# Kernel tuning notes

Hardware: AMD Instinct MI355X
Metric: run time of the kernel (lower is better)

The kernel has to match this reference:

```python
import jax, jax.numpy as jnp
import numpy as np

MAX_REL = 64  # max_relative_position (init kwarg)


def setup_inputs() -> dict:
    B, S, D, K = 8, 2048, 256, MAX_REL
    key = jax.random.key(0)
    ks = jax.random.split(key, 12)
    scale = 0.02
    return {
        "repre": jax.random.normal(ks[0], (B, S, D), jnp.float32),
        "mask": jnp.ones((B, S), jnp.int32),
        "wq1": jax.random.normal(ks[1], (D, D), jnp.float32) * scale,
        "bq1": jnp.zeros((D,), jnp.float32),
        "wk1": jax.random.normal(ks[2], (D, D), jnp.float32) * scale,
        "bk1": jnp.zeros((D,), jnp.float32),
        "rel1": jax.random.normal(ks[3], (2 * K + 1, D), jnp.float32) * scale,
        "wq2": jax.random.normal(ks[4], (D, D), jnp.float32) * scale,
        "bq2": jnp.zeros((D,), jnp.float32),
        "wk2": jax.random.normal(ks[5], (D, D), jnp.float32) * scale,
        "bk2": jnp.zeros((D,), jnp.float32),
        "rel2": jax.random.normal(ks[6], (2 * K + 1, D), jnp.float32) * scale,
    }


def _attn_logits(x, wq, bq, wk, bk, rel_emb, invalid, rel_idx):
    # Single-head relative-position attention scores (OpenNMT style):
    # query is pre-scaled by 1/sqrt(d); relative-key bias folded into scores.
    B, S, D = x.shape
    q = (x @ wq.T + bq) / jnp.sqrt(jnp.asarray(D, x.dtype))  # [B,S,D]
    k = x @ wk.T + bk                                        # [B,S,D]
    scores = jnp.einsum("bqd,bkd->bqk", q, k)               # [B,S,S]
    # relative-position term: q . rel_emb[clip(k-q)] without the [S,S,D] table
    q_rel = jnp.einsum("bqd,rd->bqr", q, rel_emb)            # [B,S,2K+1]
    idx = jnp.broadcast_to(rel_idx[None, :, :], (B, S, S))
    rel_scores = jnp.take_along_axis(q_rel, idx, axis=2)     # [B,S,S]
    scores = scores + rel_scores
    return jnp.where(invalid, jnp.asarray(-1e18, scores.dtype), scores)


def reference(repre, mask, wq1, bq1, wk1, bk1, rel1, wq2, bq2, wk2, bk2, rel2):
    B, S, D = repre.shape
    K = MAX_REL
    pos = jnp.arange(S)
    rel_idx = jnp.clip(pos[None, :] - pos[:, None], -K, K) + K  # [S,S] in [0,2K]
    # square_mask = ~(mask^T @ mask): attend only where both positions valid
    invalid = (mask[:, :, None] * mask[:, None, :]) == 0        # [B,S,S] bool
    span_st_logits = _attn_logits(repre, wq1, bq1, wk1, bk1, rel1, invalid, rel_idx)
    span_ed_logits = _attn_logits(repre, wq2, bq2, wk2, bk2, rel2, invalid, rel_idx)
    return (span_st_logits, span_ed_logits)
```

## Files before the change

### kernel.cpp

```cpp
#include <hip/hip_runtime.h>
#include <hip/hip_bf16.h>

typedef __attribute__((ext_vector_type(4))) float f32x4;
typedef __attribute__((ext_vector_type(8))) short short8;

struct bf16x4 { __hip_bfloat16 a, b, c, d; };

#define BS   8
#define SQ   2048
#define DD   256
#define KREL 64
#define NREL 129

static const size_t OFF_XBF   = 0;
static const size_t OFF_WBF   = 8388608;
static const size_t OFF_RELBF = 8912896;
static const size_t OFF_WR    = 9044992;
static const size_t OFF_CR    = 9307136;
static const size_t OFF_QK    = 9309184;
static const size_t OFF_QR    = 42863616;

struct ConvArgs {
  const float* src[7];
  __hip_bfloat16* dst[7];
  float scale[7];
  int cum4[8];
};
struct bf4 { __hip_bfloat16 a, b, c, d; };

__global__ __launch_bounds__(256) void convert_k(ConvArgs A) {
  const int idx = blockIdx.x * 256 + threadIdx.x;
  if (idx >= A.cum4[7]) return;
  int rg = 0;
  #pragma unroll
  for (int t = 1; t < 7; ++t) rg += (idx >= A.cum4[t]);
  const int local = idx - A.cum4[rg];
  const float4 v = ((const float4*)A.src[rg])[local];
  const float sc = A.scale[rg];
  bf4 o;
  o.a = __float2bfloat16(v.x * sc);
  o.b = __float2bfloat16(v.y * sc);
  o.c = __float2bfloat16(v.z * sc);
  o.d = __float2bfloat16(v.w * sc);
  ((bf4*)A.dst[rg])[local] = o;
}

__global__ __launch_bounds__(256) void wr_k(const __hip_bfloat16* __restrict__ relbf,
                                            const __hip_bfloat16* __restrict__ wbf,
                                            const float* __restrict__ bq1,
                                            const float* __restrict__ bq2,
                                            __hip_bfloat16* __restrict__ wr,
                                            float* __restrict__ cr) {
  const int r = blockIdx.x;
  const int h = blockIdx.y;
  const int e = threadIdx.x;
  const int lane = e & 63, wv = e >> 6;
  const __hip_bfloat16* rel = relbf + (size_t)h * (NREL * DD);
  const __hip_bfloat16* wq  = wbf + (size_t)h * (2 * DD * DD);
  float a0 = 0.f, a1 = 0.f, a2 = 0.f, a3 = 0.f;
  if (r < NREL) {
    #pragma unroll 4
    for (int d = 0; d < DD; d += 4) {
      a0 += __bfloat162float(rel[r * DD + d + 0]) * __bfloat162float(wq[(d + 0) * DD + e]);
      a1 += __bfloat162float(rel[r * DD + d + 1]) * __bfloat162float(wq[(d + 1) * DD + e]);
      a2 += __bfloat162float(rel[r * DD + d + 2]) * __bfloat162float(wq[(d + 2) * DD + e]);
      a3 += __bfloat162float(rel[r * DD + d + 3]) * __bfloat162float(wq[(d + 3) * DD + e]);
    }
  }
  wr[((size_t)h * DD + r) * DD + e] = __float2bfloat16((a0 + a1) + (a2 + a3));

  const float* bq = h ? bq2 : bq1;
  float p = (r < NREL) ? bq[e] * 0.0625f * __bfloat162float(rel[r * DD + e]) : 0.f;
  #pragma unroll
  for (int o = 32; o > 0; o >>= 1) p += __shfl_down(p, o, 64);
  __shared__ float wred[4];
  if (lane == 0) wred[wv] = p;
  __syncthreads();
  if (e == 0) cr[h * DD + r] = (wred[0] + wred[1]) + (wred[2] + wred[3]);
}

__device__ __forceinline__ void stage_tile(const __hip_bfloat16* __restrict__ A,
                                           const __hip_bfloat16* __restrict__ B,
                                           int rowBase, int colBase, int k0,
                                           char* As, char* Bs, int wv, int lane) {
  #pragma unroll
  for (int inst = 0; inst < 2; ++inst) {
    const int lds_off = wv * 2048 + inst * 1024;
    const int chunk = (lds_off >> 4) + lane;
    const int r  = chunk >> 2;
    const int c  = chunk & 3;
    const int kk = (c ^ ((r >> 1) & 3)) * 8;
    __builtin_amdgcn_global_load_lds(
        (const __attribute__((address_space(1))) void*)(A + (size_t)(rowBase + r) * DD + k0 + kk),
        (__attribute__((address_space(3))) void*)(As + lds_off), 16, 0, 0);
    __builtin_amdgcn_global_load_lds(
        (const __attribute__((address_space(1))) void*)(B + (size_t)(colBase + r) * DD + k0 + kk),
        (__attribute__((address_space(3))) void*)(Bs + lds_off), 16, 0, 0);
  }
}

__device__ __forceinline__ void gemm_tbuf(const __hip_bfloat16* __restrict__ A,
                                          const __hip_bfloat16* __restrict__ B,
                                          int rowBase, int colBase,
                                          char* lds,
                                          f32x4 acc[4][4]) {
  const int tid  = threadIdx.x;
  const int lane = tid & 63;
  const int wv   = tid >> 6;
  const int wrow = (wv >> 1) * 64;
  const int wcol = (wv & 1) * 64;
  const int m    = lane & 15;
  const int quad = lane >> 4;
  const int qs   = (quad ^ ((m >> 1) & 3)) * 16;

  char* As[3] = {lds,        lds + 16384, lds + 32768};
  char* Bs[3] = {lds + 8192, lds + 24576, lds + 40960};

  const f32x4 zf = {0.f, 0.f, 0.f, 0.f};
  #pragma unroll
  for (int si = 0; si < 4; ++si)
    #pragma unroll
    for (int sj = 0; sj < 4; ++sj) acc[si][sj] = zf;

  stage_tile(A, B, rowBase, colBase, 0,  As[0], Bs[0], wv, lane);
  stage_tile(A, B, rowBase, colBase, 32, As[1], Bs[1], wv, lane);

  #pragma unroll
  for (int k = 0; k < 8; ++k) {
    if (k < 7) asm volatile("s_waitcnt vmcnt(4)" ::: "memory");
    else       asm volatile("s_waitcnt vmcnt(0)" ::: "memory");
    __builtin_amdgcn_sched_barrier(0);
    __builtin_amdgcn_s_barrier();
    __builtin_amdgcn_sched_barrier(0);
    if (k < 6)
      stage_tile(A, B, rowBase, colBase, (k + 2) * 32,
                 As[(k + 2) % 3], Bs[(k + 2) % 3], wv, lane);

    const int cur = k % 3;
    short8 af[4], bf[4];
    #pragma unroll
    for (int s = 0; s < 4; ++s) {
      af[s] = *(const short8*)(As[cur] + (wrow + s * 16 + m) * 64 + qs);
      bf[s] = *(const short8*)(Bs[cur] + (wcol + s * 16 + m) * 64 + qs);
    }
    #pragma unroll
    for (int si = 0; si < 4; ++si)
      #pragma unroll
      for (int sj = 0; sj < 4; ++sj)
        acc[si][sj] = __builtin_amdgcn_mfma_f32_16x16x32_bf16(bf[sj], af[si], acc[si][sj], 0, 0, 0);
  }
}

struct QKArgs {
  const __hip_bfloat16* X;
  const __hip_bfloat16* W[6];
  const float* bias[6];
  void* out[6];
  float bscale[6];
  int isf32[6];
};

__global__ __launch_bounds__(256) void qk_k(QKArgs A) {
  __shared__ char lds[49152];
  const int flat = blockIdx.x + (blockIdx.y << 1) + (blockIdx.z << 8);
  const int swz  = (flat & 7) * 192 + (flat >> 3);
  const int colT = swz & 1;
  const int rowT = (swz >> 1) & 127;
  const int z    = swz >> 8;
  const int rowBase = rowT * 128;
  const int colBase = colT * 128;
  f32x4 acc[4][4];
  gemm_tbuf(A.X, A.W[z], rowBase, colBase, lds, acc);

  const int tid  = threadIdx.x;
  const int lane = tid & 63;
  const int wv   = tid >> 6;
  const int wrow = (wv >> 1) * 64;
  const int wcol = (wv & 1) * 64;
  const int m    = lane & 15;
  const int quad = lane >> 4;

  const float* bias = A.bias[z];
  const float bs = A.bscale[z];
  const int f32o = A.isf32[z];
  float* fo = (float*)A.out[z];
  __hip_bfloat16* bo = (__hip_bfloat16*)A.out[z];

  #pragma unroll
  for (int si = 0; si < 4; ++si) {
    const int i = rowBase + wrow + si * 16 + m;
    #pragma unroll
    for (int sj = 0; sj < 4; ++sj) {
      const int j0 = colBase + wcol + sj * 16 + quad * 4;
      const f32x4 bj = *(const f32x4*)(bias + j0);
      f32x4 v;
      #pragma unroll
      for (int r = 0; r < 4; ++r) v[r] = acc[si][sj][r] + bj[r] * bs;
      const size_t idx = (size_t)i * DD + j0;
      if (f32o) {
        *(f32x4*)(fo + idx) = v;
      } else {
        bf16x4 o;
        o.a = __float2bfloat16(v[0]);
        o.b = __float2bfloat16(v[1]);
        o.c = __float2bfloat16(v[2]);
        o.d = __float2bfloat16(v[3]);
        *(bf16x4*)(bo + idx) = o;
      }
    }
  }
}

__global__ __launch_bounds__(256) void score_k(const __hip_bfloat16* __restrict__ Q1,
                                               const __hip_bfloat16* __restrict__ K1,
                                               const float* __restrict__ QR1,
                                               const __hip_bfloat16* __restrict__ Q2,
                                               const __hip_bfloat16* __restrict__ K2,
                                               const float* __restrict__ QR2,
                                               const int* __restrict__ mask,
                                               float* __restrict__ out) {
  __shared__ char lds[49152];
  const int flat = blockIdx.x + (blockIdx.y << 4) + (blockIdx.z << 8);
  const int swz  = ((flat & 7) << 9) | (flat >> 3);
  const int colT = swz & 15;
  const int rowT = (swz >> 4) & 15;
  const int z    = swz >> 8;
  const int h = z >> 3, b = z & 7;
  const __hip_bfloat16* Q  = (h ? Q2 : Q1) + (size_t)b * SQ * DD;
  const __hip_bfloat16* Kk = (h ? K2 : K1) + (size_t)b * SQ * DD;
  const float* QR = (h ? QR2 : QR1) + (size_t)b * SQ * DD;
  const int* mk = mask + b * SQ;
  float* outp = out + (size_t)z * SQ * SQ;
  const int rowBase = rowT * 128;
  const int colBase = colT * 128;

  f32x4 acc[4][4];
  gemm_tbuf(Q, Kk, rowBase, colBase, lds, acc);

  const int tid  = threadIdx.x;
  const int lane = tid & 63;
  const int wv   = tid >> 6;
  const int wrow = (wv >> 1) * 64;
  const int wcol = (wv & 1) * 64;
  const int m    = lane & 15;
  const int quad = lane >> 4;

  const int delta = colBase - rowBase;
  const int mode = (delta >= 192) ? 1 : (delta <= -192 ? -1 : 0);

  int4 mj4[4];
  #pragma unroll
  for (int sj = 0; sj < 4; ++sj)
    mj4[sj] = *(const int4*)(mk + colBase + wcol + sj * 16 + quad * 4);

  #pragma unroll
  for (int si = 0; si < 4; ++si) {
    const int i = rowBase + wrow + si * 16 + m;
    const int mi = mk[i];
    const float* qr_row = QR + (size_t)i * DD;
    float* orow = outp + (size_t)i * SQ;
    float relc = 0.f;
    if (mode) relc = qr_row[mode == 1 ? 2 * KREL : 0];
    #pragma unroll
    for (int sj = 0; sj < 4; ++sj) {
      const int j0 = colBase + wcol + sj * 16 + quad * 4;
      f32x4 v;
      if (mode) {
        #pragma unroll
        for (int r = 0; r < 4; ++r) v[r] = acc[si][sj][r] + relc;
      } else {
        #pragma unroll
        for (int r = 0; r < 4; ++r) {
          int d = j0 + r - i;
          d = d < -KREL ? -KREL : (d > KREL ? KREL : d);
          v[r] = acc[si][sj][r] + qr_row[d + KREL];
        }
      }
      const int4 mj = mj4[sj];
      if (!(mi && mj.x)) v[0] = -1e18f;
      if (!(mi && mj.y)) v[1] = -1e18f;
      if (!(mi && mj.z)) v[2] = -1e18f;
      if (!(mi && mj.w)) v[3] = -1e18f;
      *(f32x4*)(orow + j0) = v;
    }
  }
}

extern "C" void kernel_launch(void* const* d_in, const int* in_sizes, int n_in,
                              void* d_out, int out_size, void* d_ws, size_t ws_size,
                              hipStream_t stream) {
  const float* repre = (const float*)d_in[0];
  const int*   mask  = (const int*)d_in[1];
  const float* wq1 = (const float*)d_in[2];
  const float* bq1 = (const float*)d_in[3];
  const float* wk1 = (const float*)d_in[4];
  const float* bk1 = (const float*)d_in[5];
  const float* rel1 = (const float*)d_in[6];
  const float* wq2 = (const float*)d_in[7];
  const float* bq2 = (const float*)d_in[8];
  const float* wk2 = (const float*)d_in[9];
  const float* bk2 = (const float*)d_in[10];
  const float* rel2 = (const float*)d_in[11];

  char* ws = (char*)d_ws;
  __hip_bfloat16* xbf   = (__hip_bfloat16*)(ws + OFF_XBF);
  __hip_bfloat16* wbf   = (__hip_bfloat16*)(ws + OFF_WBF);
  __hip_bfloat16* relbf = (__hip_bfloat16*)(ws + OFF_RELBF);
  __hip_bfloat16* wr    = (__hip_bfloat16*)(ws + OFF_WR);
  float*          cr    = (float*)(ws + OFF_CR);
  __hip_bfloat16* Q1 = (__hip_bfloat16*)(ws + OFF_QK);
  __hip_bfloat16* K1 = Q1 + (size_t)16384 * 256;
  __hip_bfloat16* Q2 = K1 + (size_t)16384 * 256;
  __hip_bfloat16* K2 = Q2 + (size_t)16384 * 256;
  float* QR1 = (float*)(ws + OFF_QR);
  float* QR2 = QR1 + (size_t)16384 * 256;

  ConvArgs ca;
  ca.src[0] = repre; ca.dst[0] = xbf;            ca.scale[0] = 1.f;
  ca.src[1] = wq1;   ca.dst[1] = wbf;            ca.scale[1] = 0.0625f;
  ca.src[2] = wk1;   ca.dst[2] = wbf + 65536;    ca.scale[2] = 1.f;
  ca.src[3] = wq2;   ca.dst[3] = wbf + 131072;   ca.scale[3] = 0.0625f;
  ca.src[4] = wk2;   ca.dst[4] = wbf + 196608;   ca.scale[4] = 1.f;
  ca.src[5] = rel1;  ca.dst[5] = relbf;          ca.scale[5] = 1.f;
  ca.src[6] = rel2;  ca.dst[6] = relbf + 33024;  ca.scale[6] = 1.f;
  const int sizes[7] = {4194304, 65536, 65536, 65536, 65536, 33024, 33024};
  int cum = 0;
  ca.cum4[0] = 0;
  for (int i = 0; i < 7; ++i) { cum += sizes[i] / 4; ca.cum4[i + 1] = cum; }
  const int nblk = (cum + 255) / 256;
  hipLaunchKernelGGL(convert_k, dim3(nblk), dim3(256), 0, stream, ca);

  hipLaunchKernelGGL(wr_k, dim3(256, 2), dim3(256), 0, stream, relbf, wbf, bq1, bq2, wr, cr);

  QKArgs qa;
  qa.X = xbf;
  qa.W[0] = wbf;          qa.bias[0] = bq1;      qa.bscale[0] = 0.0625f; qa.out[0] = Q1;  qa.isf32[0] = 0;
  qa.W[1] = wbf + 65536;  qa.bias[1] = bk1;      qa.bscale[1] = 1.f;     qa.out[1] = K1;  qa.isf32[1] = 0;
  qa.W[2] = wr;           qa.bias[2] = cr;       qa.bscale[2] = 1.f;     qa.out[2] = QR1; qa.isf32[2] = 1;
  qa.W[3] = wbf + 131072; qa.bias[3] = bq2;      qa.bscale[3] = 0.0625f; qa.out[3] = Q2;  qa.isf32[3] = 0;
  qa.W[4] = wbf + 196608; qa.bias[4] = bk2;      qa.bscale[4] = 1.f;     qa.out[4] = K2;  qa.isf32[4] = 0;
  qa.W[5] = wr + 65536;   qa.bias[5] = cr + 256; qa.bscale[5] = 1.f;     qa.out[5] = QR2; qa.isf32[5] = 1;
  hipLaunchKernelGGL(qk_k, dim3(2, 128, 6), dim3(256), 0, stream, qa);

  hipLaunchKernelGGL(score_k, dim3(16, 16, 16), dim3(256), 0, stream,
                     Q1, K1, QR1, Q2, K2, QR2, mask, (float*)d_out);
}
```

Baseline: 404.7 us.

## Overlap head-2 projection GEMM with head-1 score computation in combined kernel

Splits the projection kernel by head. Head-1 projections run first. A combined kernel then runs the head-2 projection GEMM tiles alongside the head-1 score tiles, and the head-2 scores run in a final launch. This fills the GPU's tail underuse of the projection stage with score work, at the cost of one extra launch and mixed block types in one grid.

After: 430.3 us. +6.3%, slower.

```diff
diff --git a/kernel.cpp b/kernel.cpp
--- a/kernel.cpp
+++ b/kernel.cpp
@@ -160,18 +160,9 @@
   int isf32[6];
 };
 
-__global__ __launch_bounds__(256) void qk_k(QKArgs A) {
-  __shared__ char lds[49152];
-  const int flat = blockIdx.x + (blockIdx.y << 1) + (blockIdx.z << 8);
-  const int swz  = (flat & 7) * 192 + (flat >> 3);
-  const int colT = swz & 1;
-  const int rowT = (swz >> 1) & 127;
-  const int z    = swz >> 8;
-  const int rowBase = rowT * 128;
-  const int colBase = colT * 128;
-  f32x4 acc[4][4];
-  gemm_tbuf(A.X, A.W[z], rowBase, colBase, lds, acc);
-
+__device__ __forceinline__ void qk_epilogue(const QKArgs& A, int z,
+                                            int rowBase, int colBase,
+                                            const f32x4 acc[4][4]) {
   const int tid  = threadIdx.x;
   const int lane = tid & 63;
   const int wv   = tid >> 6;
@@ -211,32 +202,11 @@
   }
 }
 
-__global__ __launch_bounds__(256) void score_k(const __hip_bfloat16* __restrict__ Q1,
-                                               const __hip_bfloat16* __restrict__ K1,
-                                               const float* __restrict__ QR1,
-                                               const __hip_bfloat16* __restrict__ Q2,
-                                               const __hip_bfloat16* __restrict__ K2,
-                                               const float* __restrict__ QR2,
-                                               const int* __restrict__ mask,
-                                               float* __restrict__ out) {
-  __shared__ char lds[49152];
-  const int flat = blockIdx.x + (blockIdx.y << 4) + (blockIdx.z << 8);
-  const int swz  = ((flat & 7) << 9) | (flat >> 3);
-  const int colT = swz & 15;
-  const int rowT = (swz >> 4) & 15;
-  const int z    = swz >> 8;
-  const int h = z >> 3, b = z & 7;
-  const __hip_bfloat16* Q  = (h ? Q2 : Q1) + (size_t)b * SQ * DD;
-  const __hip_bfloat16* Kk = (h ? K2 : K1) + (size_t)b * SQ * DD;
-  const float* QR = (h ? QR2 : QR1) + (size_t)b * SQ * DD;
-  const int* mk = mask + b * SQ;
-  float* outp = out + (size_t)z * SQ * SQ;
-  const int rowBase = rowT * 128;
-  const int colBase = colT * 128;
-
-  f32x4 acc[4][4];
-  gemm_tbuf(Q, Kk, rowBase, colBase, lds, acc);
-
+__device__ __forceinline__ void score_epilogue(const float* __restrict__ QR,
+                                               const int* __restrict__ mk,
+                                               float* __restrict__ outp,
+                                               int rowBase, int colBase,
+                                               const f32x4 acc[4][4]) {
   const int tid  = threadIdx.x;
   const int lane = tid & 63;
   const int wv   = tid >> 6;
@@ -286,6 +256,83 @@
   }
 }
 
+__global__ __launch_bounds__(256) void qk_k(QKArgs A, int zbase) {
+  __shared__ char lds[49152];
+  const int flat = blockIdx.x + (blockIdx.y << 1) + (blockIdx.z << 8);
+  const int swz  = (flat & 7) * 96 + (flat >> 3);
+  const int colT = swz & 1;
+  const int rowT = (swz >> 1) & 127;
+  const int z    = zbase + (swz >> 8);
+  const int rowBase = rowT * 128;
+  const int colBase = colT * 128;
+  f32x4 acc[4][4];
+  gemm_tbuf(A.X, A.W[z], rowBase, colBase, lds, acc);
+  qk_epilogue(A, z, rowBase, colBase, acc);
+}
+
+__global__ __launch_bounds__(256) void score_k(const __hip_bfloat16* __restrict__ Qh,
+                                               const __hip_bfloat16* __restrict__ Kh,
+                                               const float* __restrict__ QRh,
+                                               const int* __restrict__ mask,
+                                               float* __restrict__ outh) {
+  __shared__ char lds[49152];
+  const int flat = blockIdx.x + (blockIdx.y << 4) + (blockIdx.z << 8);
+  const int swz  = (flat & 7) * 256 + (flat >> 3);
+  const int colT = swz & 15;
+  const int rowT = (swz >> 4) & 15;
+  const int b    = swz >> 8;
+  const __hip_bfloat16* Q  = Qh + (size_t)b * SQ * DD;
+  const __hip_bfloat16* Kk = Kh + (size_t)b * SQ * DD;
+  const float* QR = QRh + (size_t)b * SQ * DD;
+  const int* mk = mask + b * SQ;
+  float* outp = outh + (size_t)b * SQ * SQ;
+  const int rowBase = rowT * 128;
+  const int colBase = colT * 128;
+  f32x4 acc[4][4];
+  gemm_tbuf(Q, Kk, rowBase, colBase, lds, acc);
+  score_epilogue(QR, mk, outp, rowBase, colBase, acc);
+}
+
+struct ComboArgs {
+  QKArgs qa;
+  const __hip_bfloat16* Q1;
+  const __hip_bfloat16* K1;
+  const float* QR1;
+  const int* mask;
+  float* out;
+};
+
+__global__ __launch_bounds__(256) void combo_k(ComboArgs C) {
+  __shared__ char lds[49152];
+  f32x4 acc[4][4];
+  if (blockIdx.x < 768) {
+    const int flat = blockIdx.x;
+    const int swz  = (flat & 7) * 96 + (flat >> 3);
+    const int colT = swz & 1;
+    const int rowT = (swz >> 1) & 127;
+    const int z    = 3 + (swz >> 8);
+    const int rowBase = rowT * 128;
+    const int colBase = colT * 128;
+    gemm_tbuf(C.qa.X, C.qa.W[z], rowBase, colBase, lds, acc);
+    qk_epilogue(C.qa, z, rowBase, colBase, acc);
+  } else {
+    const int flat = blockIdx.x - 768;
+    const int swz  = (flat & 7) * 256 + (flat >> 3);
+    const int colT = swz & 15;
+    const int rowT = (swz >> 4) & 15;
+    const int b    = swz >> 8;
+    const __hip_bfloat16* Q  = C.Q1 + (size_t)b * SQ * DD;
+    const __hip_bfloat16* Kk = C.K1 + (size_t)b * SQ * DD;
+    const float* QR = C.QR1 + (size_t)b * SQ * DD;
+    const int* mk = C.mask + b * SQ;
+    float* outp = C.out + (size_t)b * SQ * SQ;
+    const int rowBase = rowT * 128;
+    const int colBase = colT * 128;
+    gemm_tbuf(Q, Kk, rowBase, colBase, lds, acc);
+    score_epilogue(QR, mk, outp, rowBase, colBase, acc);
+  }
+}
+
 extern "C" void kernel_launch(void* const* d_in, const int* in_sizes, int n_in,
                               void* d_out, int out_size, void* d_ws, size_t ws_size,
                               hipStream_t stream) {
@@ -340,8 +387,13 @@
   qa.W[3] = wbf + 131072; qa.bias[3] = bq2;      qa.bscale[3] = 0.0625f; qa.out[3] = Q2;  qa.isf32[3] = 0;
   qa.W[4] = wbf + 196608; qa.bias[4] = bk2;      qa.bscale[4] = 1.f;     qa.out[4] = K2;  qa.isf32[4] = 0;
   qa.W[5] = wr + 65536;   qa.bias[5] = cr + 256; qa.bscale[5] = 1.f;     qa.out[5] = QR2; qa.isf32[5] = 1;
-  hipLaunchKernelGGL(qk_k, dim3(2, 128, 6), dim3(256), 0, stream, qa);
-
-  hipLaunchKernelGGL(score_k, dim3(16, 16, 16), dim3(256), 0, stream,
-                     Q1, K1, QR1, Q2, K2, QR2, mask, (float*)d_out);
-}
+  hipLaunchKernelGGL(qk_k, dim3(2, 128, 3), dim3(256), 0, stream, qa, 0);
+
+  ComboArgs cb;
+  cb.qa = qa; cb.Q1 = Q1; cb.K1 = K1; cb.QR1 = QR1; cb.mask = mask;
+  cb.out = (float*)d_out;
+  hipLaunchKernelGGL(combo_k, dim3(2816), dim3(256), 0, stream, cb);
+
+  hipLaunchKernelGGL(score_k, dim3(16, 16, 8), dim3(256), 0, stream,
+                     Q2, K2, QR2, mask, (float*)d_out + (size_t)8 * SQ * SQ);
+}
```
